# Performance work log

Measured on AMD Instinct MI355X. Metric: run time of the kernel, lower is better.

Reference implementation:

```python
import jax, jax.numpy as jnp
import numpy as np

DIM = 768
NUM_HEADS = 12
HEAD_DIM = DIM // NUM_HEADS
SCALE = HEAD_DIM ** -0.5


def setup_inputs() -> dict:
    key = jax.random.key(0)
    ks = jax.random.split(key, 7)
    B, N, C = 8, 1024, DIM
    x = jax.random.normal(ks[0], (B, N, C), dtype=jnp.float32)
    mask = jax.random.randint(ks[1], (B, N), 0, 2) > 0  # True = masked out
    qkv_w = jax.random.normal(ks[2], (3 * C, C), dtype=jnp.float32) * 0.02
    q_bias = jax.random.normal(ks[3], (C,), dtype=jnp.float32) * 0.02
    v_bias = jax.random.normal(ks[4], (C,), dtype=jnp.float32) * 0.02
    proj_w = jax.random.normal(ks[5], (C, C), dtype=jnp.float32) * 0.02
    proj_b = jax.random.normal(ks[6], (C,), dtype=jnp.float32) * 0.02
    return {"x": x, "mask": mask, "qkv_w": qkv_w, "q_bias": q_bias,
            "v_bias": v_bias, "proj_w": proj_w, "proj_b": proj_b}


def reference(x, mask, qkv_w, q_bias, v_bias, proj_w, proj_b):
    B, N, C = x.shape
    # CAE bias: concat(q_bias, zeros, v_bias) for the fused qkv projection
    qkv_bias = jnp.concatenate([q_bias, jnp.zeros_like(v_bias), v_bias])
    qkv = x @ qkv_w.T + qkv_bias  # [B, N, 3C]
    qkv = qkv.reshape(B, N, 3, NUM_HEADS, HEAD_DIM)
    q, k, v = (qkv[:, :, i].transpose(0, 2, 1, 3) for i in range(3))  # [B,H,N,hd]
    attn = jnp.einsum('bhqd,bhkd->bhqk', q * SCALE, k)  # [B,H,N,N]
    attn = jnp.where(mask[:, None, None, :], -jnp.inf, attn)
    attn = jax.nn.softmax(attn, axis=-1)
    out = jnp.einsum('bhqk,bhkd->bhqd', attn, v)  # [B,H,N,hd]
    out = out.transpose(0, 2, 1, 3).reshape(B, N, C)
    return out @ proj_w.T + proj_b
```

## Files before the change

kernel.cpp:

```cpp
#include <hip/hip_runtime.h>
#include <cstddef>
#include <cstdint>


typedef __attribute__((ext_vector_type(4))) float f32x4;
typedef __attribute__((ext_vector_type(8))) __bf16 bf16x8;
typedef __attribute__((ext_vector_type(4))) unsigned int uint4v;
typedef __attribute__((ext_vector_type(4))) unsigned short ushort4v;

#define QK_PRESCALE 0.18033688011112042f

__device__ __forceinline__ unsigned short f2bf(float f) {
  union { float f; unsigned u; } v; v.f = f;
  unsigned r = v.u + 0x7FFFu + ((v.u >> 16) & 1u);
  return (unsigned short)(r >> 16);
}

__device__ __forceinline__ void gl_lds16(const unsigned short* g, unsigned short* l) {
  __builtin_amdgcn_global_load_lds(
      (const __attribute__((address_space(1))) unsigned int*)g,
      (__attribute__((address_space(3))) unsigned int*)l, 16, 0, 0);
}

__global__ __launch_bounds__(256)
void cvt_kernel(const float* __restrict__ src, unsigned short* __restrict__ dst, int n4) {
  int i = blockIdx.x * 256 + threadIdx.x;
  if (i < n4) {
    float4 v = ((const float4*)src)[i];
    ushort4v o;
    o.x = f2bf(v.x); o.y = f2bf(v.y); o.z = f2bf(v.z); o.w = f2bf(v.w);
    ((ushort4v*)dst)[i] = o;
  }
}

__global__ __launch_bounds__(256)
void qkv_gemm(const unsigned short* __restrict__ xb, const unsigned short* __restrict__ wb,
              const float* __restrict__ qb, const float* __restrict__ vb,
              unsigned short* __restrict__ qo, unsigned short* __restrict__ ko,
              unsigned short* __restrict__ vto) {
  __shared__ __align__(16) unsigned short smem[17408];
  const int tid = threadIdx.x;
  const int lane = tid & 63, wid = tid >> 6;
  const int lm = lane & 15, lq = lane >> 4;
  const int wm = (wid & 1) * 64, wn = (wid >> 1) * 64;
  const int xsw = lm & 7;
  const int L = blockIdx.x;
  const int xcd = L & 7, s = L >> 3;
  const int m0 = (xcd * 8 + (s & 7)) * 128;
  const int n0 = (s >> 3) * 128;
  const bool sw = (n0 < 1536);
  const unsigned short* Ab = sw ? wb : xb;
  const unsigned short* Bb = sw ? xb : wb;
  const int Ao = sw ? n0 : m0;
  const int Bo = sw ? m0 : n0;
  const int srow = lane >> 3;
  const int scolsw = ((lane & 7) ^ srow) * 8;
  const unsigned short* ga = Ab + (size_t)(Ao + wid * 32 + srow) * 768 + scolsw;
  const unsigned short* gb = Bb + (size_t)(Bo + wid * 32 + srow) * 768 + scolsw;
  f32x4 acc[4][4] = {};

  for (int kt = 0; kt < 768; kt += 64) {
#pragma unroll
    for (int i = 0; i < 4; ++i) {
      gl_lds16(ga + kt + (size_t)i * 8 * 768, &smem[(wid * 32 + i * 8) * 64]);
      gl_lds16(gb + kt + (size_t)i * 8 * 768, &smem[8192 + (wid * 32 + i * 8) * 64]);
    }
    __syncthreads();
#pragma unroll
    for (int ks = 0; ks < 2; ++ks) {
      bf16x8 af[4], bf[4];
#pragma unroll
      for (int i = 0; i < 4; ++i)
        af[i] = *(const bf16x8*)&smem[(wm + i * 16 + lm) * 64 + (((ks * 4 + lq) ^ xsw) * 8)];
#pragma unroll
      for (int i = 0; i < 4; ++i)
        bf[i] = *(const bf16x8*)&smem[8192 + (wn + i * 16 + lm) * 64 + (((ks * 4 + lq) ^ xsw) * 8)];
#pragma unroll
      for (int mi = 0; mi < 4; ++mi)
#pragma unroll
        for (int ni = 0; ni < 4; ++ni)
          acc[mi][ni] = __builtin_amdgcn_mfma_f32_16x16x32_bf16(af[mi], bf[ni], acc[mi][ni], 0, 0, 0);
    }
    __syncthreads();
  }

  if (sw) {
    const int which = (n0 >= 768) ? 1 : 0;
    const int within0 = n0 - which * 768;
#pragma unroll
    for (int mi = 0; mi < 4; ++mi) {
      int d0 = wm + mi * 16 + lq * 4;
      f32x4 bias4 = {0.f, 0.f, 0.f, 0.f};
      if (which == 0) bias4 = *(const f32x4*)&qb[within0 + d0];
#pragma unroll
      for (int ni = 0; ni < 4; ++ni) {
        int tokl = wn + ni * 16 + lm;
        ushort4v pk;
        if (which == 0) {
          pk.x = f2bf((acc[mi][ni][0] + bias4[0]) * QK_PRESCALE);
          pk.y = f2bf((acc[mi][ni][1] + bias4[1]) * QK_PRESCALE);
          pk.z = f2bf((acc[mi][ni][2] + bias4[2]) * QK_PRESCALE);
          pk.w = f2bf((acc[mi][ni][3] + bias4[3]) * QK_PRESCALE);
        } else {
          pk.x = f2bf(acc[mi][ni][0]); pk.y = f2bf(acc[mi][ni][1]);
          pk.z = f2bf(acc[mi][ni][2]); pk.w = f2bf(acc[mi][ni][3]);
        }
        *(ushort4v*)&smem[tokl * 136 + d0] = pk;
      }
    }
    __syncthreads();
    {
      int tok = tid >> 1, half = tid & 1;
      int b = m0 >> 10;
      int tokg = (m0 & 1023) + tok;
      int hh = (within0 >> 6) + half;
      unsigned short* dst = which ? ko : qo;
      size_t base = (((size_t)(b * 12 + hh)) * 1024 + tokg) * 64;
      const unsigned short* srcr = &smem[tok * 136 + half * 64];
#pragma unroll
      for (int j = 0; j < 8; ++j)
        *(uint4v*)&dst[base + j * 8] = *(const uint4v*)&srcr[j * 8];
    }
  } else {
    const int within0 = n0 - 1536;
#pragma unroll
    for (int mi = 0; mi < 4; ++mi) {
      int tok0 = wm + mi * 16 + lq * 4;
#pragma unroll
      for (int ni = 0; ni < 4; ++ni) {
        int dl = wn + ni * 16 + lm;
        float bias = vb[within0 + dl];
        ushort4v pk;
        pk.x = f2bf(acc[mi][ni][0] + bias);
        pk.y = f2bf(acc[mi][ni][1] + bias);
        pk.z = f2bf(acc[mi][ni][2] + bias);
        pk.w = f2bf(acc[mi][ni][3] + bias);
        *(ushort4v*)&smem[dl * 136 + tok0] = pk;
      }
    }
    __syncthreads();
    {
      int dl = tid >> 1, halft = tid & 1;
      int within = within0 + dl;
      int hh = within >> 6, d = within & 63;
      int b = m0 >> 10;
      int tokg0 = (m0 & 1023) + halft * 64;
      size_t base = (((size_t)(b * 12 + hh)) * 64 + d) * 1024 + tokg0;
      const unsigned short* srcr = &smem[dl * 136 + halft * 64];
#pragma unroll
      for (int j = 0; j < 8; ++j)
        *(uint4v*)&vto[base + j * 8] = *(const uint4v*)&srcr[j * 8];
    }
  }
}

__global__ __launch_bounds__(256)
void attn_mfma(const unsigned short* __restrict__ q, const unsigned short* __restrict__ k,
               const unsigned short* __restrict__ vt, const int* __restrict__ mask,
               unsigned short* __restrict__ ao) {
  __shared__ unsigned short ks_s[64 * 64];
  __shared__ unsigned short vs_s[64 * 64];
  __shared__ unsigned short ps[4][32 * 72];
  __shared__ float mkl[64];
  const int tid = threadIdx.x;
  const int lane = tid & 63, wid = tid >> 6;
  const int lm = lane & 15, lq = lane >> 4;
  const int xsw = lm & 7;
  const int L = blockIdx.x;
  const int xcd = L & 7, s = L >> 3;
  const int bh = xcd * 12 + s / 8;
  const int qt = s % 8;
  const int bb = bh / 12, hh = bh % 12;
  const unsigned short* qp = q + (size_t)bh * 65536;
  const unsigned short* kp = k + (size_t)bh * 65536;
  const unsigned short* vp = vt + (size_t)bh * 65536;
  const int* mp = mask + bb * 1024;
  const int q0 = qt * 128 + wid * 32;
  const int srow = lane >> 3;
  const int scolsw = ((lane & 7) ^ srow) * 8;
  const unsigned short* gk = kp + (size_t)(wid * 16 + srow) * 64 + scolsw;
  const unsigned short* gv = vp + (size_t)(wid * 16 + srow) * 1024 + scolsw;

  bf16x8 qf[2][2];
#pragma unroll
  for (int mi = 0; mi < 2; ++mi)
#pragma unroll
    for (int ks2 = 0; ks2 < 2; ++ks2)
      qf[mi][ks2] = *(const bf16x8*)&qp[(size_t)(q0 + mi * 16 + lm) * 64 + ks2 * 32 + lq * 8];
  bf16x8 ones;
#pragma unroll
  for (int i = 0; i < 8; ++i) ones[i] = (__bf16)1.0f;

  f32x4 o_acc[2][4] = {};
  f32x4 l_acc[2] = {};

  for (int kt = 0; kt < 16; ++kt) {
    __syncthreads();
#pragma unroll
    for (int i = 0; i < 2; ++i) {
      gl_lds16(gk + (size_t)kt * 4096 + (size_t)i * 8 * 64, &ks_s[(wid * 16 + i * 8) * 64]);
      gl_lds16(gv + (size_t)kt * 64 + (size_t)i * 8 * 1024, &vs_s[(wid * 16 + i * 8) * 64]);
    }
    if (tid < 64) mkl[tid] = mp[kt * 64 + tid] ? -1e30f : 0.0f;
    __syncthreads();

    f32x4 st[4][2] = {};
#pragma unroll
    for (int ks2 = 0; ks2 < 2; ++ks2) {
      bf16x8 kf[4];
#pragma unroll
      for (int nt = 0; nt < 4; ++nt)
        kf[nt] = *(const bf16x8*)&ks_s[(nt * 16 + lm) * 64 + (((ks2 * 4 + lq) ^ xsw) * 8)];
#pragma unroll
      for (int nt = 0; nt < 4; ++nt)
#pragma unroll
        for (int mi = 0; mi < 2; ++mi)
          st[nt][mi] = __builtin_amdgcn_mfma_f32_16x16x32_bf16(kf[nt], qf[mi][ks2], st[nt][mi], 0, 0, 0);
    }

#pragma unroll
    for (int nt = 0; nt < 4; ++nt) {
      f32x4 mv4 = *(const f32x4*)&mkl[nt * 16 + lq * 4];
#pragma unroll
      for (int mi = 0; mi < 2; ++mi) {
        ushort4v pk;
        pk.x = f2bf(exp2f(st[nt][mi][0] + mv4[0]));
        pk.y = f2bf(exp2f(st[nt][mi][1] + mv4[1]));
        pk.z = f2bf(exp2f(st[nt][mi][2] + mv4[2]));
        pk.w = f2bf(exp2f(st[nt][mi][3] + mv4[3]));
        *(ushort4v*)&ps[wid][(mi * 16 + lm) * 72 + nt * 16 + lq * 4] = pk;
      }
    }

#pragma unroll
    for (int ks2 = 0; ks2 < 2; ++ks2) {
      bf16x8 pf[2], vf[4];
#pragma unroll
      for (int mi = 0; mi < 2; ++mi)
        pf[mi] = *(const bf16x8*)&ps[wid][(mi * 16 + lm) * 72 + ks2 * 32 + lq * 8];
#pragma unroll
      for (int nt = 0; nt < 4; ++nt)
        vf[nt] = *(const bf16x8*)&vs_s[(nt * 16 + lm) * 64 + (((ks2 * 4 + lq) ^ xsw) * 8)];
#pragma unroll
      for (int mi = 0; mi < 2; ++mi) {
#pragma unroll
        for (int nt = 0; nt < 4; ++nt)
          o_acc[mi][nt] = __builtin_amdgcn_mfma_f32_16x16x32_bf16(pf[mi], vf[nt], o_acc[mi][nt], 0, 0, 0);
        l_acc[mi] = __builtin_amdgcn_mfma_f32_16x16x32_bf16(pf[mi], ones, l_acc[mi], 0, 0, 0);
      }
    }
  }

#pragma unroll
  for (int mi = 0; mi < 2; ++mi) {
#pragma unroll
    for (int r = 0; r < 4; ++r) {
      float inv = 1.0f / l_acc[mi][r];
      int tok = q0 + mi * 16 + lq * 4 + r;
#pragma unroll
      for (int nt = 0; nt < 4; ++nt)
        ao[(size_t)(bb * 1024 + tok) * 768 + hh * 64 + nt * 16 + lm] = f2bf(o_acc[mi][nt][r] * inv);
    }
  }
}

__global__ __launch_bounds__(256)
void proj_gemm(const unsigned short* __restrict__ ab, const unsigned short* __restrict__ wb,
               const float* __restrict__ pb, float* __restrict__ out) {
  __shared__ unsigned short as[128 * 64];
  __shared__ unsigned short bs[128 * 64];
  const int tid = threadIdx.x;
  const int lane = tid & 63, wid = tid >> 6;
  const int lm = lane & 15, lq = lane >> 4;
  const int xsw = lm & 7;
  const int wm = (wid & 1) * 64, wn = (wid >> 1) * 64;
  const int L = blockIdx.x;
  const int xcd = L & 7, s = L >> 3;
  const int m0 = (xcd * 8 + s / 6) * 128;
  const int n0 = (s % 6) * 128;
  const int srow = lane >> 3;
  const int scolsw = ((lane & 7) ^ srow) * 8;
  const unsigned short* ga = wb + (size_t)(n0 + wid * 32 + srow) * 768 + scolsw;
  const unsigned short* gb = ab + (size_t)(m0 + wid * 32 + srow) * 768 + scolsw;
  f32x4 acc[4][4] = {};
  for (int kt = 0; kt < 768; kt += 64) {
#pragma unroll
    for (int i = 0; i < 4; ++i) {
      gl_lds16(ga + kt + (size_t)i * 8 * 768, &as[(wid * 32 + i * 8) * 64]);
      gl_lds16(gb + kt + (size_t)i * 8 * 768, &bs[(wid * 32 + i * 8) * 64]);
    }
    __syncthreads();
#pragma unroll
    for (int ks = 0; ks < 2; ++ks) {
      bf16x8 af[4], bf[4];
#pragma unroll
      for (int i = 0; i < 4; ++i)
        af[i] = *(const bf16x8*)&as[(wm + i * 16 + lm) * 64 + (((ks * 4 + lq) ^ xsw) * 8)];
#pragma unroll
      for (int i = 0; i < 4; ++i)
        bf[i] = *(const bf16x8*)&bs[(wn + i * 16 + lm) * 64 + (((ks * 4 + lq) ^ xsw) * 8)];
#pragma unroll
      for (int mi = 0; mi < 4; ++mi)
#pragma unroll
        for (int ni = 0; ni < 4; ++ni)
          acc[mi][ni] = __builtin_amdgcn_mfma_f32_16x16x32_bf16(af[mi], bf[ni], acc[mi][ni], 0, 0, 0);
    }
    __syncthreads();
  }
#pragma unroll
  for (int mi = 0; mi < 4; ++mi) {
    int gn0 = n0 + wm + mi * 16 + lq * 4;
    f32x4 bias4 = *(const f32x4*)&pb[gn0];
#pragma unroll
    for (int ni = 0; ni < 4; ++ni) {
      int gm = m0 + wn + ni * 16 + lm;
      f32x4 o;
      o[0] = acc[mi][ni][0] + bias4[0];
      o[1] = acc[mi][ni][1] + bias4[1];
      o[2] = acc[mi][ni][2] + bias4[2];
      o[3] = acc[mi][ni][3] + bias4[3];
      *(f32x4*)&out[(size_t)gm * 768 + gn0] = o;
    }
  }
}

extern "C" void kernel_launch(void* const* d_in, const int* in_sizes, int n_in,
                              void* d_out, int out_size, void* d_ws, size_t ws_size,
                              hipStream_t stream) {
  const float* x      = (const float*)d_in[0];
  const int*   mask   = (const int*)d_in[1];
  const float* qkv_w  = (const float*)d_in[2];
  const float* q_bias = (const float*)d_in[3];
  const float* v_bias = (const float*)d_in[4];
  const float* proj_w = (const float*)d_in[5];
  const float* proj_b = (const float*)d_in[6];
  float* out = (float*)d_out;
  unsigned short* p = (unsigned short*)d_ws;
  unsigned short* xb     = p;              p += 6291456;
  unsigned short* wqkvb  = p;              p += 1769472;
  unsigned short* wprojb = p;              p += 589824;
  unsigned short* qo     = p;              p += 6291456;
  unsigned short* ko     = p;              p += 6291456;
  unsigned short* vto    = p;              p += 6291456;
  unsigned short* ao     = p;

  cvt_kernel<<<6144, 256, 0, stream>>>(x, xb, 1572864);
  cvt_kernel<<<1728, 256, 0, stream>>>(qkv_w, wqkvb, 442368);
  cvt_kernel<<<576, 256, 0, stream>>>(proj_w, wprojb, 147456);
  qkv_gemm<<<1152, 256, 0, stream>>>(xb, wqkvb, q_bias, v_bias, qo, ko, vto);
  attn_mfma<<<768, 256, 0, stream>>>(qo, ko, vto, mask, ao);
  proj_gemm<<<384, 256, 0, stream>>>(ao, wprojb, proj_b, out);
}
```

Measured before the change: 216.0 us.

## Double-buffer K/V tiles in attention and use cheaper packed bf16 conversion

The attention kernel now double-buffers its K, V and mask tiles in LDS, issuing the global-to-LDS loads for the next key tile before computing on the current one, with one barrier per iteration instead of two. The aim is to hide global load latency behind the MFMA work. Separately, float-to-bf16 conversion switches from round-to-nearest-even to a simpler round-half-up and packs pairs with a byte permute, cutting ALU work in all kernels. The cost is twice the K/V LDS footprint, which may lower occupancy, and slightly different rounding.

```diff
diff --git a/kernel.cpp b/kernel.cpp
--- a/kernel.cpp
+++ b/kernel.cpp
@@ -6,14 +6,18 @@
 typedef __attribute__((ext_vector_type(4))) float f32x4;
 typedef __attribute__((ext_vector_type(8))) __bf16 bf16x8;
 typedef __attribute__((ext_vector_type(4))) unsigned int uint4v;
+typedef __attribute__((ext_vector_type(2))) unsigned int uint2v;
 typedef __attribute__((ext_vector_type(4))) unsigned short ushort4v;
 
 #define QK_PRESCALE 0.18033688011112042f
 
 __device__ __forceinline__ unsigned short f2bf(float f) {
-  union { float f; unsigned u; } v; v.f = f;
-  unsigned r = v.u + 0x7FFFu + ((v.u >> 16) & 1u);
-  return (unsigned short)(r >> 16);
+  return (unsigned short)((__float_as_uint(f) + 0x8000u) >> 16);
+}
+__device__ __forceinline__ unsigned int pack2bf(float flo, float fhi) {
+  unsigned ulo = __float_as_uint(flo) + 0x8000u;
+  unsigned uhi = __float_as_uint(fhi) + 0x8000u;
+  return __builtin_amdgcn_perm(uhi, ulo, 0x07060302);
 }
 
 __device__ __forceinline__ void gl_lds16(const unsigned short* g, unsigned short* l) {
@@ -27,9 +31,10 @@
   int i = blockIdx.x * 256 + threadIdx.x;
   if (i < n4) {
     float4 v = ((const float4*)src)[i];
-    ushort4v o;
-    o.x = f2bf(v.x); o.y = f2bf(v.y); o.z = f2bf(v.z); o.w = f2bf(v.w);
-    ((ushort4v*)dst)[i] = o;
+    uint2v o;
+    o.x = pack2bf(v.x, v.y);
+    o.y = pack2bf(v.z, v.w);
+    ((uint2v*)dst)[i] = o;
   }
 }
 
@@ -95,17 +100,17 @@
 #pragma unroll
       for (int ni = 0; ni < 4; ++ni) {
         int tokl = wn + ni * 16 + lm;
-        ushort4v pk;
+        uint2v pk;
         if (which == 0) {
-          pk.x = f2bf((acc[mi][ni][0] + bias4[0]) * QK_PRESCALE);
-          pk.y = f2bf((acc[mi][ni][1] + bias4[1]) * QK_PRESCALE);
-          pk.z = f2bf((acc[mi][ni][2] + bias4[2]) * QK_PRESCALE);
-          pk.w = f2bf((acc[mi][ni][3] + bias4[3]) * QK_PRESCALE);
+          pk.x = pack2bf((acc[mi][ni][0] + bias4[0]) * QK_PRESCALE,
+                         (acc[mi][ni][1] + bias4[1]) * QK_PRESCALE);
+          pk.y = pack2bf((acc[mi][ni][2] + bias4[2]) * QK_PRESCALE,
+                         (acc[mi][ni][3] + bias4[3]) * QK_PRESCALE);
         } else {
-          pk.x = f2bf(acc[mi][ni][0]); pk.y = f2bf(acc[mi][ni][1]);
-          pk.z = f2bf(acc[mi][ni][2]); pk.w = f2bf(acc[mi][ni][3]);
+          pk.x = pack2bf(acc[mi][ni][0], acc[mi][ni][1]);
+          pk.y = pack2bf(acc[mi][ni][2], acc[mi][ni][3]);
         }
-        *(ushort4v*)&smem[tokl * 136 + d0] = pk;
+        *(uint2v*)&smem[tokl * 136 + d0] = pk;
       }
     }
     __syncthreads();
@@ -130,12 +135,10 @@
       for (int ni = 0; ni < 4; ++ni) {
         int dl = wn + ni * 16 + lm;
         float bias = vb[within0 + dl];
-        ushort4v pk;
-        pk.x = f2bf(acc[mi][ni][0] + bias);
-        pk.y = f2bf(acc[mi][ni][1] + bias);
-        pk.z = f2bf(acc[mi][ni][2] + bias);
-        pk.w = f2bf(acc[mi][ni][3] + bias);
-        *(ushort4v*)&smem[dl * 136 + tok0] = pk;
+        uint2v pk;
+        pk.x = pack2bf(acc[mi][ni][0] + bias, acc[mi][ni][1] + bias);
+        pk.y = pack2bf(acc[mi][ni][2] + bias, acc[mi][ni][3] + bias);
+        *(uint2v*)&smem[dl * 136 + tok0] = pk;
       }
     }
     __syncthreads();
@@ -158,10 +161,10 @@
 void attn_mfma(const unsigned short* __restrict__ q, const unsigned short* __restrict__ k,
                const unsigned short* __restrict__ vt, const int* __restrict__ mask,
                unsigned short* __restrict__ ao) {
-  __shared__ unsigned short ks_s[64 * 64];
-  __shared__ unsigned short vs_s[64 * 64];
+  __shared__ unsigned short ks_s[2 * 4096];
+  __shared__ unsigned short vs_s[2 * 4096];
   __shared__ unsigned short ps[4][32 * 72];
-  __shared__ float mkl[64];
+  __shared__ float mkl[2][64];
   const int tid = threadIdx.x;
   const int lane = tid & 63, wid = tid >> 6;
   const int lm = lane & 15, lq = lane >> 4;
@@ -194,15 +197,26 @@
   f32x4 o_acc[2][4] = {};
   f32x4 l_acc[2] = {};
 
+#pragma unroll
+  for (int i = 0; i < 2; ++i) {
+    gl_lds16(gk + (size_t)i * 8 * 64, &ks_s[(wid * 16 + i * 8) * 64]);
+    gl_lds16(gv + (size_t)i * 8 * 1024, &vs_s[(wid * 16 + i * 8) * 64]);
+  }
+  if (tid < 64) mkl[0][tid] = mp[tid] ? -1e30f : 0.0f;
+  __syncthreads();
+
   for (int kt = 0; kt < 16; ++kt) {
-    __syncthreads();
-#pragma unroll
-    for (int i = 0; i < 2; ++i) {
-      gl_lds16(gk + (size_t)kt * 4096 + (size_t)i * 8 * 64, &ks_s[(wid * 16 + i * 8) * 64]);
-      gl_lds16(gv + (size_t)kt * 64 + (size_t)i * 8 * 1024, &vs_s[(wid * 16 + i * 8) * 64]);
-    }
-    if (tid < 64) mkl[tid] = mp[kt * 64 + tid] ? -1e30f : 0.0f;
-    __syncthreads();
+    const int cur = kt & 1, nxt = cur ^ 1;
+    if (kt < 15) {
+#pragma unroll
+      for (int i = 0; i < 2; ++i) {
+        gl_lds16(gk + (size_t)(kt + 1) * 4096 + (size_t)i * 8 * 64,
+                 &ks_s[nxt * 4096 + (wid * 16 + i * 8) * 64]);
+        gl_lds16(gv + (size_t)(kt + 1) * 64 + (size_t)i * 8 * 1024,
+                 &vs_s[nxt * 4096 + (wid * 16 + i * 8) * 64]);
+      }
+      if (tid < 64) mkl[nxt][tid] = mp[(kt + 1) * 64 + tid] ? -1e30f : 0.0f;
+    }
 
     f32x4 st[4][2] = {};
 #pragma unroll
@@ -210,7 +224,7 @@
       bf16x8 kf[4];
 #pragma unroll
       for (int nt = 0; nt < 4; ++nt)
-        kf[nt] = *(const bf16x8*)&ks_s[(nt * 16 + lm) * 64 + (((ks2 * 4 + lq) ^ xsw) * 8)];
+        kf[nt] = *(const bf16x8*)&ks_s[cur * 4096 + (nt * 16 + lm) * 64 + (((ks2 * 4 + lq) ^ xsw) * 8)];
 #pragma unroll
       for (int nt = 0; nt < 4; ++nt)
 #pragma unroll
@@ -220,15 +234,13 @@
 
 #pragma unroll
     for (int nt = 0; nt < 4; ++nt) {
-      f32x4 mv4 = *(const f32x4*)&mkl[nt * 16 + lq * 4];
+      f32x4 mv4 = *(const f32x4*)&mkl[cur][nt * 16 + lq * 4];
 #pragma unroll
       for (int mi = 0; mi < 2; ++mi) {
-        ushort4v pk;
-        pk.x = f2bf(exp2f(st[nt][mi][0] + mv4[0]));
-        pk.y = f2bf(exp2f(st[nt][mi][1] + mv4[1]));
-        pk.z = f2bf(exp2f(st[nt][mi][2] + mv4[2]));
-        pk.w = f2bf(exp2f(st[nt][mi][3] + mv4[3]));
-        *(ushort4v*)&ps[wid][(mi * 16 + lm) * 72 + nt * 16 + lq * 4] = pk;
+        uint2v pk;
+        pk.x = pack2bf(exp2f(st[nt][mi][0] + mv4[0]), exp2f(st[nt][mi][1] + mv4[1]));
+        pk.y = pack2bf(exp2f(st[nt][mi][2] + mv4[2]), exp2f(st[nt][mi][3] + mv4[3]));
+        *(uint2v*)&ps[wid][(mi * 16 + lm) * 72 + nt * 16 + lq * 4] = pk;
       }
     }
 
@@ -240,7 +252,7 @@
         pf[mi] = *(const bf16x8*)&ps[wid][(mi * 16 + lm) * 72 + ks2 * 32 + lq * 8];
 #pragma unroll
       for (int nt = 0; nt < 4; ++nt)
-        vf[nt] = *(const bf16x8*)&vs_s[(nt * 16 + lm) * 64 + (((ks2 * 4 + lq) ^ xsw) * 8)];
+        vf[nt] = *(const bf16x8*)&vs_s[cur * 4096 + (nt * 16 + lm) * 64 + (((ks2 * 4 + lq) ^ xsw) * 8)];
 #pragma unroll
       for (int mi = 0; mi < 2; ++mi) {
 #pragma unroll
@@ -249,6 +261,7 @@
         l_acc[mi] = __builtin_amdgcn_mfma_f32_16x16x32_bf16(pf[mi], ones, l_acc[mi], 0, 0, 0);
       }
     }
+    __syncthreads();
   }
 
 #pragma unroll
```

Result: slower. 223.7 us (+3.5%).
